# Performance work log

Measured on AMD Instinct MI355X. Metric: run time of the kernel, lower is better.

The kernel has to match this reference:

```python
import jax, jax.numpy as jnp
import numpy as np

S = 4          # number of species / per-species sub-modules
CUTOFF = 5.2


def _routed_mlp(feat, W, b, species_, activate=True):
    # Species-routed MLP: equivalent to per-species index_select -> m_i -> index_add.
    # Compute all species branches vectorized, then select with one-hot mask.
    h = jnp.einsum('ni,sio->nso', feat, W) + b            # [N, S, out]
    if activate:
        h = jax.nn.gelu(h)
    onehot = jax.nn.one_hot(species_, S, dtype=feat.dtype)  # [N, S]; -1 -> all-zero row
    return jnp.einsum('nso,ns->no', h, onehot)            # [N, out]


def _smooth_cutoff(d, rc):
    x = jnp.clip(d / rc, 0.0, 1.0 - 1e-6)
    f = jnp.exp(1.0 - 1.0 / (1.0 - x * x))
    return jnp.where(d < rc, f, 0.0)


def setup_inputs() -> dict:
    key = jax.random.key(0)
    ks = jax.random.split(key, 12)
    B, A, AEV, MO, NO, P = 256, 128, 1008, 256, 128, 262144
    N = B * A
    FIN = MO + NO  # 384
    species = jax.random.randint(ks[0], (B, A), 0, S, dtype=jnp.int32)
    aev = jax.random.normal(ks[1], (B, A, AEV), dtype=jnp.float32)
    atom_index12 = jax.random.randint(ks[2], (2, P), 0, N, dtype=jnp.int32)
    distances = jax.random.uniform(ks[3], (P,), dtype=jnp.float32) * CUTOFF
    total_charges = jax.random.randint(ks[4], (B,), -2, 3).astype(jnp.float32)

    def w(k, shape, fan_in):
        return jax.random.normal(k, shape, dtype=jnp.float32) / np.sqrt(fan_in)

    Wm0 = w(ks[5], (S, AEV, MO), AEV); bm0 = jnp.zeros((S, MO), jnp.float32)
    Wn0 = w(ks[6], (S, MO, NO), MO);   bn0 = jnp.zeros((S, NO), jnp.float32)
    Wm1 = w(ks[7], (S, FIN, MO), FIN); bm1 = jnp.zeros((S, MO), jnp.float32)
    Wn1 = w(ks[8], (S, MO, NO), MO);   bn1 = jnp.zeros((S, NO), jnp.float32)
    Wf  = w(ks[9], (S, FIN, 1), FIN);  bf  = jnp.zeros((S, 1), jnp.float32)
    return dict(species=species, aev=aev, atom_index12=atom_index12,
                distances=distances, total_charges=total_charges,
                Wm0=Wm0, bm0=bm0, Wn0=Wn0, bn0=bn0,
                Wm1=Wm1, bm1=bm1, Wn1=Wn1, bn1=bn1,
                Wf=Wf, bf=bf,
                factor=jnp.float32(1.0), prefactor=jnp.float32(1.0))


def reference(species, aev, atom_index12, distances, total_charges,
              Wm0, bm0, Wn0, bn0, Wm1, bm1, Wn1, bn1, Wf, bf,
              factor, prefactor):
    B, A = species.shape
    species_ = species.reshape(-1)                 # [N]
    feat = aev.reshape(-1, aev.shape[-1])          # [N, AEV]

    # ExpDistanceDecay * smooth cutoff, shared by every pass
    decay = (prefactor ** 2) * jnp.exp(-(factor ** 2) * distances) \
            * _smooth_cutoff(distances, CUTOFF)    # [P]
    idx_flat = atom_index12.reshape(-1)            # [2P] scatter targets
    idx_flip = atom_index12[::-1].reshape(-1)      # [2P] gather sources (flipud)
    decay2 = jnp.tile(decay, 2)                    # [2P]

    for (Wm, bm, Wn, bn) in ((Wm0, bm0, Wn0, bn0), (Wm1, bm1, Wn1, bn1)):
        internal = _routed_mlp(feat, Wm, bm, species_)     # [N, MO]
        neigh = _routed_mlp(internal, Wn, bn, species_)    # [N, NO]
        msgs = neigh[idx_flip] * decay2[:, None]           # [2P, NO]
        merged = jnp.zeros_like(neigh).at[idx_flat].add(msgs)
        feat = jnp.concatenate([internal, merged], axis=-1)  # [N, MO+NO]

    pre = _routed_mlp(feat, Wf, bf, species_, activate=False)[:, 0].reshape(B, A)

    dummy_mask = species != -1
    n_real = dummy_mask.sum(-1, keepdims=True).astype(pre.dtype)
    charges = pre + (total_charges - pre.sum(-1))[:, None] / n_real
    charges = jnp.where(dummy_mask, charges, 0.0)
    return species, charges, pre
```

## Files before the change

kernel.cpp:

```cpp
#include <hip/hip_runtime.h>
#include <hip/hip_bf16.h>
#include <math.h>

constexpr int S_  = 4;
constexpr int MO  = 256;
constexpr int NO  = 128;
constexpr int FIN = 384;
#define CUTOFF_F 5.2f

typedef short bf16x8 __attribute__((ext_vector_type(8)));
typedef float f32x16 __attribute__((ext_vector_type(16)));

__device__ __forceinline__ float gelu_tanh(float x) {
    float u = 0.7978845608028654f * (x + 0.044715f * x * x * x);
    return 0.5f * x * (1.0f + tanhf(u));
}
__device__ __forceinline__ unsigned short f2bf(float x) {
    unsigned u = __float_as_uint(x);
    u = (u + 0x7fffu + ((u >> 16) & 1u)) >> 16;
    return (unsigned short)u;
}
__device__ __forceinline__ float bf2f(unsigned short h) {
    return __uint_as_float(((unsigned)h) << 16);
}
__device__ __forceinline__ float decay_of(float d, float fa, float pf) {
    float x = fminf(fmaxf(d / CUTOFF_F, 0.0f), 1.0f - 1e-6f);
    float f = expf(1.0f - 1.0f / (1.0f - x * x));
    float w = (d < CUTOFF_F) ? f : 0.0f;
    return pf * pf * expf(-(fa * fa) * d) * w;
}

__global__ void species_hist(const int* __restrict__ sp, int* __restrict__ bhist, int N) {
    __shared__ int h[S_];
    int t = threadIdx.x, b = blockIdx.x;
    if (t < S_) h[t] = 0;
    __syncthreads();
    int i = b * 256 + t;
    if (i < N) {
        int s = sp[i];
        if (s >= 0 && s < S_) atomicAdd(&h[s], 1);
    }
    __syncthreads();
    if (t < S_) bhist[b * 4 + t] = h[t];
}
__global__ void species_scan(const int* __restrict__ bhist, int* __restrict__ cnt,
                             int* __restrict__ pbase, int nb) {
    if (threadIdx.x != 0) return;
    int tot[S_];
    for (int s = 0; s < S_; ++s) {
        int sum = 0;
        for (int b = 0; b < nb; ++b) sum += bhist[b * 4 + s];
        tot[s] = sum;
    }
    int off = 0;
    for (int s = 0; s < S_; ++s) { cnt[s] = tot[s]; cnt[4 + s] = off; off += tot[s]; }
    for (int s = 0; s < S_; ++s) {
        int run = cnt[4 + s];
        for (int b = 0; b < nb; ++b) { pbase[b * 4 + s] = run; run += bhist[b * 4 + s]; }
    }
}
__global__ void species_fill(const int* __restrict__ sp, const int* __restrict__ pbase,
                             int* __restrict__ perm, int N) {
    __shared__ int cur[S_];
    int t = threadIdx.x, b = blockIdx.x;
    if (t < S_) cur[t] = pbase[b * 4 + t];
    __syncthreads();
    int i = b * 256 + t;
    if (i < N) {
        int s = sp[i];
        if (s >= 0 && s < S_) {
            int pos = atomicAdd(&cur[s], 1);
            perm[pos] = i;
        }
    }
}

__global__ void edge_count(const int* __restrict__ ai, int* __restrict__ degree, int P2) {
    int e = blockIdx.x * blockDim.x + threadIdx.x;
    if (e < P2) atomicAdd(&degree[ai[e]], 1);
}
__global__ void scan_rowptr(const int* __restrict__ degree, int* __restrict__ rowptr,
                            int* __restrict__ cursor, int N) {
    __shared__ int lds[1024];
    int t = threadIdx.x;
    int per = N / 1024;
    int base = t * per;
    int sum = 0;
    for (int i = 0; i < per; ++i) sum += degree[base + i];
    lds[t] = sum;
    __syncthreads();
    int v = sum;
    for (int ofs = 1; ofs < 1024; ofs <<= 1) {
        int add = (t >= ofs) ? lds[t - ofs] : 0;
        __syncthreads();
        v += add;
        lds[t] = v;
        __syncthreads();
    }
    int run = v - sum;
    for (int i = 0; i < per; ++i) {
        int d = degree[base + i];
        rowptr[base + i] = run;
        cursor[base + i] = run;
        run += d;
    }
    if (t == 1023) rowptr[N] = run;
}
__global__ void edge_fill(const int* __restrict__ ai, const float* __restrict__ dist,
                          const float* __restrict__ fa_, const float* __restrict__ pf_,
                          int* __restrict__ cursor, int* __restrict__ col,
                          float* __restrict__ wgt, int P) {
    int e = blockIdx.x * blockDim.x + threadIdx.x;
    if (e >= 2 * P) return;
    int p = (e < P) ? e : e - P;
    int dst = ai[e];
    int src = (e < P) ? ai[P + p] : ai[p];
    int pos = atomicAdd(&cursor[dst], 1);
    col[pos] = src;
    wgt[pos] = decay_of(dist[p], fa_[0], pf_[0]);
}

__global__ void cast_aev(const float* __restrict__ in, unsigned short* __restrict__ outb, int total4) {
    int i = blockIdx.x * blockDim.x + threadIdx.x;
    if (i >= total4) return;
    float4 v = ((const float4*)in)[i];
    ushort4 o; o.x = f2bf(v.x); o.y = f2bf(v.y); o.z = f2bf(v.z); o.w = f2bf(v.w);
    ((ushort4*)outb)[i] = o;
}

__global__ void transpose_cast(const float* __restrict__ W, unsigned short* __restrict__ Wt,
                               int K, int NC) {
    __shared__ float tile[32][33];
    int s = blockIdx.z;
    int nb = blockIdx.x * 32, kb = blockIdx.y * 32;
    int tx = threadIdx.x & 31, ty = threadIdx.x >> 5;
    const float* Wb = W + (size_t)s * K * NC;
    unsigned short* Wo = Wt + (size_t)s * NC * K;
#pragma unroll
    for (int i = 0; i < 4; ++i) {
        int k = kb + ty + i * 8;
        tile[ty + i * 8][tx] = (k < K) ? Wb[(size_t)k * NC + nb + tx] : 0.0f;
    }
    __syncthreads();
#pragma unroll
    for (int i = 0; i < 4; ++i) {
        int n = nb + ty + i * 8;
        int k = kb + tx;
        if (k < K) Wo[(size_t)n * K + k] = f2bf(tile[tx][ty + i * 8]);
    }
}

template<int K, int NC, bool ACT>
__launch_bounds__(256, 2)
__global__ void mfma_gemm(const unsigned short* __restrict__ A, int lda,
                          const unsigned short* __restrict__ Wt,
                          const float* __restrict__ bias,
                          unsigned short* __restrict__ C, int ldc,
                          const int* __restrict__ cnt, const int* __restrict__ perm) {
    const int s = blockIdx.z;
    const int count = cnt[s];
    const int row0 = blockIdx.y * 64;
    if (row0 >= count) return;
    const int off = cnt[4 + s];
    const int c0 = blockIdx.x * 128;

    __shared__ unsigned short As[64 * 40];
    __shared__ unsigned short Bs[128 * 40];
    __shared__ int rix[64];

    const int t = threadIdx.x;
    const int lane = t & 63, wave = t >> 6;
    const int wm = wave >> 1, wn = wave & 1;
    const int l31 = lane & 31, lhi = lane >> 5;

    if (t < 64) {
        int ri = row0 + t;
        rix[t] = (ri < count) ? perm[off + ri] : -1;
    }
    __syncthreads();

    const int ra = t >> 2, qa = t & 3;
    const int rbr = t >> 1, hb = t & 1;
    const int gA = rix[ra];
    const unsigned short* Arow = (gA >= 0) ? (A + (size_t)gA * lda) : nullptr;
    const unsigned short* wrow = Wt + ((size_t)s * NC + c0 + rbr) * K;

    f32x16 acc0 = {}, acc1 = {};
    const uint4 z4 = {0, 0, 0, 0};

    for (int k0 = 0; k0 < K; k0 += 32) {
        const int ka = k0 + qa * 8;
        uint4 av = z4;
        if (ka < K && Arow) av = *(const uint4*)(Arow + ka);
        const int kb = k0 + hb * 16;
        uint4 b0 = z4, b1 = z4;
        if (kb < K) {
            const uint4* q = (const uint4*)(wrow + kb);
            b0 = q[0]; b1 = q[1];
        }
        __syncthreads();
        *(uint4*)(&As[ra * 40 + qa * 8]) = av;
        *(uint4*)(&Bs[rbr * 40 + hb * 16])     = b0;
        *(uint4*)(&Bs[rbr * 40 + hb * 16 + 8]) = b1;
        __syncthreads();
#pragma unroll
        for (int ks = 0; ks < 2; ++ks) {
            const int ch = (ks * 2 + lhi) * 8;
            bf16x8 fa  = *(const bf16x8*)(&As[(wm * 32 + l31) * 40 + ch]);
            bf16x8 fb0 = *(const bf16x8*)(&Bs[(wn * 64 +  0 + l31) * 40 + ch]);
            bf16x8 fb1 = *(const bf16x8*)(&Bs[(wn * 64 + 32 + l31) * 40 + ch]);
            acc0 = __builtin_amdgcn_mfma_f32_32x32x16_bf16(fa, fb0, acc0, 0, 0, 0);
            acc1 = __builtin_amdgcn_mfma_f32_32x32x16_bf16(fa, fb1, acc1, 0, 0, 0);
        }
    }

    const float* bp = bias + s * NC;
    auto store = [&](const f32x16& vv, int fn) {
        int col = c0 + wn * 64 + fn * 32 + l31;
        float bia = bp[col];
#pragma unroll
        for (int reg = 0; reg < 16; ++reg) {
            int frow = (reg & 3) + 8 * (reg >> 2) + 4 * lhi;
            int r = wm * 32 + frow;
            int g = rix[r];
            if (g >= 0) {
                float x = vv[reg] + bia;
                if (ACT) x = gelu_tanh(x);
                C[(size_t)g * ldc + col] = f2bf(x);
            }
        }
    };
    store(acc0, 0); store(acc1, 1);
}

template<int K, bool ACT>
__launch_bounds__(256, 2)
__global__ void mfma_gemm32(const unsigned short* __restrict__ A, int lda,
                            const unsigned short* __restrict__ Wt,
                            const float* __restrict__ bias,
                            unsigned short* __restrict__ C, int ldc,
                            const int* __restrict__ cnt, const int* __restrict__ perm) {
    const int s = blockIdx.z;
    const int count = cnt[s];
    const int row0 = blockIdx.y * 32;
    if (row0 >= count) return;
    const int off = cnt[4 + s];
    constexpr int NC = 128;

    __shared__ unsigned short As[32 * 40];
    __shared__ unsigned short Bs[128 * 40];
    __shared__ int rix[32];

    const int t = threadIdx.x;
    const int lane = t & 63, wave = t >> 6;
    const int l31 = lane & 31, lhi = lane >> 5;

    if (t < 32) {
        int ri = row0 + t;
        rix[t] = (ri < count) ? perm[off + ri] : -1;
    }
    __syncthreads();

    const int ra = t >> 3, qa = t & 7;
    const int rbr = t >> 1, hb = t & 1;
    const int gA = rix[ra];
    const unsigned short* Arow = (gA >= 0) ? (A + (size_t)gA * lda) : nullptr;
    const unsigned short* wrow = Wt + ((size_t)s * NC + rbr) * K;

    f32x16 acc = {};
    const uint4 z4 = {0, 0, 0, 0};
    const uint2 z2 = {0, 0};

    for (int k0 = 0; k0 < K; k0 += 32) {
        const int ka = k0 + qa * 4;
        uint2 av = z2;
        if (ka < K && Arow) av = *(const uint2*)(Arow + ka);
        const int kb = k0 + hb * 16;
        uint4 b0 = z4, b1 = z4;
        if (kb < K) {
            const uint4* q = (const uint4*)(wrow + kb);
            b0 = q[0]; b1 = q[1];
        }
        __syncthreads();
        *(uint2*)(&As[ra * 40 + qa * 4]) = av;
        *(uint4*)(&Bs[rbr * 40 + hb * 16])     = b0;
        *(uint4*)(&Bs[rbr * 40 + hb * 16 + 8]) = b1;
        __syncthreads();
#pragma unroll
        for (int ks = 0; ks < 2; ++ks) {
            const int ch = (ks * 2 + lhi) * 8;
            bf16x8 fa = *(const bf16x8*)(&As[l31 * 40 + ch]);
            bf16x8 fb = *(const bf16x8*)(&Bs[(wave * 32 + l31) * 40 + ch]);
            acc = __builtin_amdgcn_mfma_f32_32x32x16_bf16(fa, fb, acc, 0, 0, 0);
        }
    }

    const float* bp = bias + s * NC;
    int col = wave * 32 + l31;
    float bia = bp[col];
#pragma unroll
    for (int reg = 0; reg < 16; ++reg) {
        int frow = (reg & 3) + 8 * (reg >> 2) + 4 * lhi;
        int g = rix[frow];
        if (g >= 0) {
            float x = acc[reg] + bia;
            if (ACT) x = gelu_tanh(x);
            C[(size_t)g * ldc + col] = f2bf(x);
        }
    }
}

__global__ void gather_rows0(const unsigned short* __restrict__ neigh,
                             const int* __restrict__ rowptr, const int* __restrict__ col,
                             const float* __restrict__ wgt,
                             unsigned short* __restrict__ featout) {
    int row = blockIdx.x * 4 + (threadIdx.x >> 6);
    int lane = threadIdx.x & 63;
    int b = rowptr[row], e = rowptr[row + 1];
    int j = lane * 2;
    float a0 = 0.f, a1 = 0.f, c0 = 0.f, c1 = 0.f;
    int i = b;
    for (; i + 3 < e; i += 4) {
        int s0 = col[i], s1 = col[i + 1], s2 = col[i + 2], s3 = col[i + 3];
        float w0 = wgt[i], w1 = wgt[i + 1], w2 = wgt[i + 2], w3 = wgt[i + 3];
        unsigned p0 = *(const unsigned*)(neigh + (size_t)s0 * NO + j);
        unsigned p1 = *(const unsigned*)(neigh + (size_t)s1 * NO + j);
        unsigned p2 = *(const unsigned*)(neigh + (size_t)s2 * NO + j);
        unsigned p3 = *(const unsigned*)(neigh + (size_t)s3 * NO + j);
        a0 += bf2f((unsigned short)(p0 & 0xffffu)) * w0 + bf2f((unsigned short)(p2 & 0xffffu)) * w2;
        a1 += bf2f((unsigned short)(p0 >> 16)) * w0 + bf2f((unsigned short)(p2 >> 16)) * w2;
        c0 += bf2f((unsigned short)(p1 & 0xffffu)) * w1 + bf2f((unsigned short)(p3 & 0xffffu)) * w3;
        c1 += bf2f((unsigned short)(p1 >> 16)) * w1 + bf2f((unsigned short)(p3 >> 16)) * w3;
    }
    for (; i < e; ++i) {
        int s0 = col[i];
        float w0 = wgt[i];
        unsigned p0 = *(const unsigned*)(neigh + (size_t)s0 * NO + j);
        a0 += bf2f((unsigned short)(p0 & 0xffffu)) * w0;
        a1 += bf2f((unsigned short)(p0 >> 16)) * w0;
    }
    a0 += c0; a1 += c1;
    unsigned short o0 = f2bf(a0), o1 = f2bf(a1);
    *(unsigned*)(featout + (size_t)row * FIN + MO + j) = ((unsigned)o1 << 16) | (unsigned)o0;
}

__global__ void gather_final(const unsigned short* __restrict__ neigh,
                             const int* __restrict__ rowptr, const int* __restrict__ col,
                             const float* __restrict__ wgt,
                             const unsigned short* __restrict__ int1,
                             const float* __restrict__ Wf, const float* __restrict__ bfb,
                             const int* __restrict__ species, float* __restrict__ out, int N) {
    int w = blockIdx.x * 4 + (threadIdx.x >> 6);
    int lane = threadIdx.x & 63;
    int s = species[w];
    float acc = 0.0f;
    if (s >= 0) {
        const float* wp = Wf + (size_t)s * FIN;
        int b = rowptr[w], e = rowptr[w + 1];
        int j = lane * 2;
        float a0 = 0.f, a1 = 0.f, c0 = 0.f, c1 = 0.f;
        int i = b;
        for (; i + 3 < e; i += 4) {
            int s0 = col[i], s1 = col[i + 1], s2 = col[i + 2], s3 = col[i + 3];
            float w0 = wgt[i], w1 = wgt[i + 1], w2 = wgt[i + 2], w3 = wgt[i + 3];
            unsigned p0 = *(const unsigned*)(neigh + (size_t)s0 * NO + j);
            unsigned p1 = *(const unsigned*)(neigh + (size_t)s1 * NO + j);
            unsigned p2 = *(const unsigned*)(neigh + (size_t)s2 * NO + j);
            unsigned p3 = *(const unsigned*)(neigh + (size_t)s3 * NO + j);
            a0 += bf2f((unsigned short)(p0 & 0xffffu)) * w0 + bf2f((unsigned short)(p2 & 0xffffu)) * w2;
            a1 += bf2f((unsigned short)(p0 >> 16)) * w0 + bf2f((unsigned short)(p2 >> 16)) * w2;
            c0 += bf2f((unsigned short)(p1 & 0xffffu)) * w1 + bf2f((unsigned short)(p3 & 0xffffu)) * w3;
            c1 += bf2f((unsigned short)(p1 >> 16)) * w1 + bf2f((unsigned short)(p3 >> 16)) * w3;
        }
        for (; i < e; ++i) {
            int s0 = col[i];
            float w0 = wgt[i];
            unsigned p0 = *(const unsigned*)(neigh + (size_t)s0 * NO + j);
            a0 += bf2f((unsigned short)(p0 & 0xffffu)) * w0;
            a1 += bf2f((unsigned short)(p0 >> 16)) * w0;
        }
        a0 += c0; a1 += c1;
        acc = a0 * wp[MO + j] + a1 * wp[MO + j + 1];
        const unsigned short* ip = int1 + (size_t)w * MO + lane * 4;
        ushort4 iv = *(const ushort4*)ip;
        const float* wq = wp + lane * 4;
        acc += bf2f(iv.x) * wq[0] + bf2f(iv.y) * wq[1] + bf2f(iv.z) * wq[2] + bf2f(iv.w) * wq[3];
    }
    for (int o = 32; o > 0; o >>= 1) acc += __shfl_down(acc, o, 64);
    if (lane == 0) {
        float pre = (s >= 0) ? (acc + bfb[s]) : 0.0f;
        out[2 * (size_t)N + w] = pre;
        out[w] = (float)s;
    }
}

__global__ void charges_kernel(const float* __restrict__ pre_buf, const int* __restrict__ species,
                               const float* __restrict__ tc, float* __restrict__ out, int N, int A) {
    int b = blockIdx.x;
    int a = threadIdx.x;
    int idx = b * A + a;
    float pre = pre_buf[idx];
    int sp = species[idx];
    bool mask = (sp != -1);
    float v = pre;
    int c = mask ? 1 : 0;
    for (int o = 32; o > 0; o >>= 1) {
        v += __shfl_down(v, o, 64);
        c += __shfl_down(c, o, 64);
    }
    __shared__ float ssum[2];
    __shared__ int scnt[2];
    int wid = threadIdx.x >> 6;
    if ((threadIdx.x & 63) == 0) { ssum[wid] = v; scnt[wid] = c; }
    __syncthreads();
    float total = ssum[0] + ssum[1];
    int nreal = scnt[0] + scnt[1];
    float ch = pre + (tc[b] - total) / (float)max(nreal, 1);
    out[(size_t)N + idx] = mask ? ch : 0.0f;
}

extern "C" void kernel_launch(void* const* d_in, const int* in_sizes, int n_in,
                              void* d_out, int out_size, void* d_ws, size_t ws_size,
                              hipStream_t stream) {
    const int*   species = (const int*)d_in[0];
    const float* aev     = (const float*)d_in[1];
    const int*   ai      = (const int*)d_in[2];
    const float* dist    = (const float*)d_in[3];
    const float* tc      = (const float*)d_in[4];
    const float* Wm0 = (const float*)d_in[5];  const float* bm0 = (const float*)d_in[6];
    const float* Wn0 = (const float*)d_in[7];  const float* bn0 = (const float*)d_in[8];
    const float* Wm1 = (const float*)d_in[9];  const float* bm1 = (const float*)d_in[10];
    const float* Wn1 = (const float*)d_in[11]; const float* bn1 = (const float*)d_in[12];
    const float* Wf  = (const float*)d_in[13]; const float* bf  = (const float*)d_in[14];
    const float* factor    = (const float*)d_in[15];
    const float* prefactor = (const float*)d_in[16];

    const int N   = in_sizes[0];
    const int AEV = in_sizes[1] / N;
    const int P   = in_sizes[3];
    const int B   = in_sizes[4];
    const int A   = N / B;

    float* out = (float*)d_out;

    char* base = (char*)d_ws;
    size_t o = 0;
    auto take = [&](size_t bytes) -> char* {
        o = (o + 255) & ~(size_t)255;
        char* p = base + o; o += bytes; return p;
    };
    unsigned short* feat1_bf = (unsigned short*)take((size_t)N * FIN * 2);
    unsigned short* int1_bf  = (unsigned short*)take((size_t)N * MO * 2);
    char* region             = take((size_t)N * AEV * 2);
    unsigned short* aev_bf   = (unsigned short*)region;
    unsigned short* neigh_bf = (unsigned short*)region;
    size_t roff = ((size_t)N * NO * 2 + 255) & ~(size_t)255;
    int* rowptr = (int*)(region + roff);  roff += (size_t)(N + 1) * 4; roff = (roff + 255) & ~(size_t)255;
    int* cursor = (int*)(region + roff);  roff += (size_t)N * 4;       roff = (roff + 255) & ~(size_t)255;
    int* degree = (int*)(region + roff);  roff += (size_t)N * 4;       roff = (roff + 255) & ~(size_t)255;
    int* ecol   = (int*)(region + roff);  roff += (size_t)2 * P * 4;   roff = (roff + 255) & ~(size_t)255;
    float* ewgt = (float*)(region + roff);
    unsigned short* Wm0t = (unsigned short*)take((size_t)S_ * MO * AEV * 2);
    unsigned short* Wn0t = (unsigned short*)take((size_t)S_ * NO * MO * 2);
    unsigned short* Wm1t = (unsigned short*)take((size_t)S_ * MO * FIN * 2);
    unsigned short* Wn1t = (unsigned short*)take((size_t)S_ * NO * MO * 2);
    int* perm  = (int*)take((size_t)N * 4);
    int* cnt   = (int*)take(64);
    const int nb = (N + 255) / 256;
    int* bhist = (int*)take((size_t)nb * 4 * 4);
    int* pbase = (int*)take((size_t)nb * 4 * 4);

    species_hist<<<nb, 256, 0, stream>>>(species, bhist, N);
    species_scan<<<1, 64, 0, stream>>>(bhist, cnt, pbase, nb);
    species_fill<<<nb, 256, 0, stream>>>(species, pbase, perm, N);

    const int tot4 = N * (AEV / 4);
    cast_aev<<<(tot4 + 255) / 256, 256, 0, stream>>>(aev, aev_bf, tot4);
    transpose_cast<<<dim3(MO / 32, (AEV + 31) / 32, S_), 256, 0, stream>>>(Wm0, Wm0t, AEV, MO);
    transpose_cast<<<dim3(NO / 32, MO / 32, S_), 256, 0, stream>>>(Wn0, Wn0t, MO, NO);
    transpose_cast<<<dim3(MO / 32, FIN / 32, S_), 256, 0, stream>>>(Wm1, Wm1t, FIN, MO);
    transpose_cast<<<dim3(NO / 32, MO / 32, S_), 256, 0, stream>>>(Wn1, Wn1t, MO, NO);

    const int rb  = (N + 63) / 64;
    const int rb32 = (N + 31) / 32;

    mfma_gemm<1008, 256, true><<<dim3(2, rb, S_), 256, 0, stream>>>(
        aev_bf, AEV, Wm0t, bm0, feat1_bf, FIN, cnt, perm);

    hipMemsetAsync(degree, 0, (size_t)N * 4, stream);
    edge_count<<<(2 * P + 255) / 256, 256, 0, stream>>>(ai, degree, 2 * P);
    scan_rowptr<<<1, 1024, 0, stream>>>(degree, rowptr, cursor, N);
    edge_fill<<<(2 * P + 255) / 256, 256, 0, stream>>>(ai, dist, factor, prefactor,
                                                       cursor, ecol, ewgt, P);

    mfma_gemm32<256, true><<<dim3(1, rb32, S_), 256, 0, stream>>>(
        feat1_bf, FIN, Wn0t, bn0, neigh_bf, NO, cnt, perm);
    gather_rows0<<<N / 4, 256, 0, stream>>>(neigh_bf, rowptr, ecol, ewgt, feat1_bf);

    mfma_gemm<384, 256, true><<<dim3(2, rb, S_), 256, 0, stream>>>(
        feat1_bf, FIN, Wm1t, bm1, int1_bf, MO, cnt, perm);
    mfma_gemm32<256, true><<<dim3(1, rb32, S_), 256, 0, stream>>>(
        int1_bf, MO, Wn1t, bn1, neigh_bf, NO, cnt, perm);

    gather_final<<<N / 4, 256, 0, stream>>>(
        neigh_bf, rowptr, ecol, ewgt, int1_bf, Wf, bf, species, out, N);
    charges_kernel<<<B, A, 0, stream>>>(out + 2 * (size_t)N, species, tc, out, N, A);
}
```

Measured before the change: 610.9 us.

## Store all activations in species-sorted padded row order to drop indirect GEMM rows

Rows are permuted once into species-sorted order, with each species segment padded to a multiple of 64, while AEV is cast to bf16. From then on the GEMMs read contiguous rows and pick the species from the tile's offset, with no per-row perm indirection, and the grid drops its per-species z dimension so no blocks exit early. The edge CSR is rebuilt in permuted indices, and the final kernel scatters results back to original atom order. This removes scattered row gathers and wasted blocks, at the cost of an extra inverse-permutation array, padded buffers and extra memsets.

```diff
diff --git a/kernel.cpp b/kernel.cpp
--- a/kernel.cpp
+++ b/kernel.cpp
@@ -53,14 +53,19 @@
         tot[s] = sum;
     }
     int off = 0;
-    for (int s = 0; s < S_; ++s) { cnt[s] = tot[s]; cnt[4 + s] = off; off += tot[s]; }
+    for (int s = 0; s < S_; ++s) {
+        cnt[s] = tot[s];
+        cnt[4 + s] = off;
+        off += ((tot[s] + 63) / 64) * 64;
+    }
+    cnt[8] = off;
     for (int s = 0; s < S_; ++s) {
         int run = cnt[4 + s];
         for (int b = 0; b < nb; ++b) { pbase[b * 4 + s] = run; run += bhist[b * 4 + s]; }
     }
 }
 __global__ void species_fill(const int* __restrict__ sp, const int* __restrict__ pbase,
-                             int* __restrict__ perm, int N) {
+                             int* __restrict__ perm, int* __restrict__ inv_perm, int N) {
     __shared__ int cur[S_];
     int t = threadIdx.x, b = blockIdx.x;
     if (t < S_) cur[t] = pbase[b * 4 + t];
@@ -71,19 +76,40 @@
         if (s >= 0 && s < S_) {
             int pos = atomicAdd(&cur[s], 1);
             perm[pos] = i;
-        }
-    }
-}
-
-__global__ void edge_count(const int* __restrict__ ai, int* __restrict__ degree, int P2) {
+            inv_perm[i] = pos;
+        }
+    }
+}
+
+__global__ void cast_gather(const float* __restrict__ aev, const int* __restrict__ perm,
+                            unsigned short* __restrict__ outb, int AEV) {
+    int row = blockIdx.x;
+    int t = threadIdx.x;
+    if (t * 4 >= AEV) return;
+    int atom = perm[row];
+    ushort4 o;
+    if (atom >= 0) {
+        float4 v = *(const float4*)(aev + (size_t)atom * AEV + t * 4);
+        o.x = f2bf(v.x); o.y = f2bf(v.y); o.z = f2bf(v.z); o.w = f2bf(v.w);
+    } else {
+        o.x = o.y = o.z = o.w = 0;
+    }
+    *(ushort4*)(outb + (size_t)row * AEV + t * 4) = o;
+}
+
+__global__ void edge_count(const int* __restrict__ ai, const int* __restrict__ inv_perm,
+                           int* __restrict__ degree, int P2) {
     int e = blockIdx.x * blockDim.x + threadIdx.x;
-    if (e < P2) atomicAdd(&degree[ai[e]], 1);
+    if (e < P2) {
+        int d = inv_perm[ai[e]];
+        if (d >= 0) atomicAdd(&degree[d], 1);
+    }
 }
 __global__ void scan_rowptr(const int* __restrict__ degree, int* __restrict__ rowptr,
-                            int* __restrict__ cursor, int N) {
+                            int* __restrict__ cursor, int NSCAN) {
     __shared__ int lds[1024];
     int t = threadIdx.x;
-    int per = N / 1024;
+    int per = NSCAN / 1024;
     int base = t * per;
     int sum = 0;
     for (int i = 0; i < per; ++i) sum += degree[base + i];
@@ -104,28 +130,22 @@
         cursor[base + i] = run;
         run += d;
     }
-    if (t == 1023) rowptr[N] = run;
+    if (t == 1023) rowptr[NSCAN] = run;
 }
 __global__ void edge_fill(const int* __restrict__ ai, const float* __restrict__ dist,
                           const float* __restrict__ fa_, const float* __restrict__ pf_,
+                          const int* __restrict__ inv_perm,
                           int* __restrict__ cursor, int* __restrict__ col,
                           float* __restrict__ wgt, int P) {
     int e = blockIdx.x * blockDim.x + threadIdx.x;
     if (e >= 2 * P) return;
     int p = (e < P) ? e : e - P;
-    int dst = ai[e];
-    int src = (e < P) ? ai[P + p] : ai[p];
+    int dst = inv_perm[ai[e]];
+    if (dst < 0) return;
+    int src = inv_perm[(e < P) ? ai[P + p] : ai[p]];
     int pos = atomicAdd(&cursor[dst], 1);
-    col[pos] = src;
-    wgt[pos] = decay_of(dist[p], fa_[0], pf_[0]);
-}
-
-__global__ void cast_aev(const float* __restrict__ in, unsigned short* __restrict__ outb, int total4) {
-    int i = blockIdx.x * blockDim.x + threadIdx.x;
-    if (i >= total4) return;
-    float4 v = ((const float4*)in)[i];
-    ushort4 o; o.x = f2bf(v.x); o.y = f2bf(v.y); o.z = f2bf(v.z); o.w = f2bf(v.w);
-    ((ushort4*)outb)[i] = o;
+    col[pos] = (src >= 0) ? src : 0;
+    wgt[pos] = (src >= 0) ? decay_of(dist[p], fa_[0], pf_[0]) : 0.0f;
 }
 
 __global__ void transpose_cast(const float* __restrict__ W, unsigned short* __restrict__ Wt,
@@ -156,33 +176,23 @@
                           const unsigned short* __restrict__ Wt,
                           const float* __restrict__ bias,
                           unsigned short* __restrict__ C, int ldc,
-                          const int* __restrict__ cnt, const int* __restrict__ perm) {
-    const int s = blockIdx.z;
-    const int count = cnt[s];
+                          const int* __restrict__ cnt) {
     const int row0 = blockIdx.y * 64;
-    if (row0 >= count) return;
-    const int off = cnt[4 + s];
+    if (row0 >= cnt[8]) return;
+    const int s = (row0 >= cnt[5]) + (row0 >= cnt[6]) + (row0 >= cnt[7]);
     const int c0 = blockIdx.x * 128;
 
     __shared__ unsigned short As[64 * 40];
     __shared__ unsigned short Bs[128 * 40];
-    __shared__ int rix[64];
 
     const int t = threadIdx.x;
     const int lane = t & 63, wave = t >> 6;
     const int wm = wave >> 1, wn = wave & 1;
     const int l31 = lane & 31, lhi = lane >> 5;
 
-    if (t < 64) {
-        int ri = row0 + t;
-        rix[t] = (ri < count) ? perm[off + ri] : -1;
-    }
-    __syncthreads();
-
     const int ra = t >> 2, qa = t & 3;
     const int rbr = t >> 1, hb = t & 1;
-    const int gA = rix[ra];
-    const unsigned short* Arow = (gA >= 0) ? (A + (size_t)gA * lda) : nullptr;
+    const unsigned short* Arow = A + (size_t)(row0 + ra) * lda;
     const unsigned short* wrow = Wt + ((size_t)s * NC + c0 + rbr) * K;
 
     f32x16 acc0 = {}, acc1 = {};
@@ -191,7 +201,7 @@
     for (int k0 = 0; k0 < K; k0 += 32) {
         const int ka = k0 + qa * 8;
         uint4 av = z4;
-        if (ka < K && Arow) av = *(const uint4*)(Arow + ka);
+        if (ka < K) av = *(const uint4*)(Arow + ka);
         const int kb = k0 + hb * 16;
         uint4 b0 = z4, b1 = z4;
         if (kb < K) {
@@ -221,13 +231,10 @@
 #pragma unroll
         for (int reg = 0; reg < 16; ++reg) {
             int frow = (reg & 3) + 8 * (reg >> 2) + 4 * lhi;
-            int r = wm * 32 + frow;
-            int g = rix[r];
-            if (g >= 0) {
-                float x = vv[reg] + bia;
-                if (ACT) x = gelu_tanh(x);
-                C[(size_t)g * ldc + col] = f2bf(x);
-            }
+            int r = row0 + wm * 32 + frow;
+            float x = vv[reg] + bia;
+            if (ACT) x = gelu_tanh(x);
+            C[(size_t)r * ldc + col] = f2bf(x);
         }
     };
     store(acc0, 0); store(acc1, 1);
@@ -239,32 +246,22 @@
                             const unsigned short* __restrict__ Wt,
                             const float* __restrict__ bias,
                             unsigned short* __restrict__ C, int ldc,
-                            const int* __restrict__ cnt, const int* __restrict__ perm) {
-    const int s = blockIdx.z;
-    const int count = cnt[s];
+                            const int* __restrict__ cnt) {
     const int row0 = blockIdx.y * 32;
-    if (row0 >= count) return;
-    const int off = cnt[4 + s];
+    if (row0 >= cnt[8]) return;
+    const int s = (row0 >= cnt[5]) + (row0 >= cnt[6]) + (row0 >= cnt[7]);
     constexpr int NC = 128;
 
     __shared__ unsigned short As[32 * 40];
     __shared__ unsigned short Bs[128 * 40];
-    __shared__ int rix[32];
 
     const int t = threadIdx.x;
     const int lane = t & 63, wave = t >> 6;
     const int l31 = lane & 31, lhi = lane >> 5;
 
-    if (t < 32) {
-        int ri = row0 + t;
-        rix[t] = (ri < count) ? perm[off + ri] : -1;
-    }
-    __syncthreads();
-
     const int ra = t >> 3, qa = t & 7;
     const int rbr = t >> 1, hb = t & 1;
-    const int gA = rix[ra];
-    const unsigned short* Arow = (gA >= 0) ? (A + (size_t)gA * lda) : nullptr;
+    const unsigned short* Arow = A + (size_t)(row0 + ra) * lda;
     const unsigned short* wrow = Wt + ((size_t)s * NC + rbr) * K;
 
     f32x16 acc = {};
@@ -274,7 +271,7 @@
     for (int k0 = 0; k0 < K; k0 += 32) {
         const int ka = k0 + qa * 4;
         uint2 av = z2;
-        if (ka < K && Arow) av = *(const uint2*)(Arow + ka);
+        if (ka < K) av = *(const uint2*)(Arow + ka);
         const int kb = k0 + hb * 16;
         uint4 b0 = z4, b1 = z4;
         if (kb < K) {
@@ -301,12 +298,10 @@
 #pragma unroll
     for (int reg = 0; reg < 16; ++reg) {
         int frow = (reg & 3) + 8 * (reg >> 2) + 4 * lhi;
-        int g = rix[frow];
-        if (g >= 0) {
-            float x = acc[reg] + bia;
-            if (ACT) x = gelu_tanh(x);
-            C[(size_t)g * ldc + col] = f2bf(x);
-        }
+        int r = row0 + frow;
+        float x = acc[reg] + bia;
+        if (ACT) x = gelu_tanh(x);
+        C[(size_t)r * ldc + col] = f2bf(x);
     }
 }
 
@@ -348,11 +343,15 @@
                              const int* __restrict__ rowptr, const int* __restrict__ col,
                              const float* __restrict__ wgt,
                              const unsigned short* __restrict__ int1,
+                             const int* __restrict__ perm,
+                             const int* __restrict__ species,
                              const float* __restrict__ Wf, const float* __restrict__ bfb,
-                             const int* __restrict__ species, float* __restrict__ out, int N) {
+                             float* __restrict__ out, int N) {
     int w = blockIdx.x * 4 + (threadIdx.x >> 6);
     int lane = threadIdx.x & 63;
-    int s = species[w];
+    int atom = perm[w];
+    if (atom < 0) return;
+    int s = species[atom];
     float acc = 0.0f;
     if (s >= 0) {
         const float* wp = Wf + (size_t)s * FIN;
@@ -389,8 +388,8 @@
     for (int o = 32; o > 0; o >>= 1) acc += __shfl_down(acc, o, 64);
     if (lane == 0) {
         float pre = (s >= 0) ? (acc + bfb[s]) : 0.0f;
-        out[2 * (size_t)N + w] = pre;
-        out[w] = (float)s;
+        out[2 * (size_t)N + atom] = pre;
+        out[atom] = (float)s;
     }
 }
 
@@ -441,6 +440,9 @@
     const int B   = in_sizes[4];
     const int A   = N / B;
 
+    const int NPAD  = N + 256;
+    const int NSCAN = ((NPAD + 1023) / 1024) * 1024;
+
     float* out = (float*)d_out;
 
     char* base = (char*)d_ws;
@@ -449,60 +451,62 @@
         o = (o + 255) & ~(size_t)255;
         char* p = base + o; o += bytes; return p;
     };
-    unsigned short* feat1_bf = (unsigned short*)take((size_t)N * FIN * 2);
-    unsigned short* int1_bf  = (unsigned short*)take((size_t)N * MO * 2);
-    char* region             = take((size_t)N * AEV * 2);
+    unsigned short* feat1_bf = (unsigned short*)take((size_t)NPAD * FIN * 2);
+    unsigned short* int1_bf  = (unsigned short*)take((size_t)NPAD * MO * 2);
+    char* region             = take((size_t)NPAD * AEV * 2);
     unsigned short* aev_bf   = (unsigned short*)region;
     unsigned short* neigh_bf = (unsigned short*)region;
-    size_t roff = ((size_t)N * NO * 2 + 255) & ~(size_t)255;
-    int* rowptr = (int*)(region + roff);  roff += (size_t)(N + 1) * 4; roff = (roff + 255) & ~(size_t)255;
-    int* cursor = (int*)(region + roff);  roff += (size_t)N * 4;       roff = (roff + 255) & ~(size_t)255;
-    int* degree = (int*)(region + roff);  roff += (size_t)N * 4;       roff = (roff + 255) & ~(size_t)255;
-    int* ecol   = (int*)(region + roff);  roff += (size_t)2 * P * 4;   roff = (roff + 255) & ~(size_t)255;
+    size_t roff = ((size_t)NPAD * NO * 2 + 255) & ~(size_t)255;
+    int* rowptr = (int*)(region + roff);  roff += (size_t)(NSCAN + 1) * 4; roff = (roff + 255) & ~(size_t)255;
+    int* cursor = (int*)(region + roff);  roff += (size_t)NSCAN * 4;       roff = (roff + 255) & ~(size_t)255;
+    int* degree = (int*)(region + roff);  roff += (size_t)NSCAN * 4;       roff = (roff + 255) & ~(size_t)255;
+    int* ecol   = (int*)(region + roff);  roff += (size_t)2 * P * 4;       roff = (roff + 255) & ~(size_t)255;
     float* ewgt = (float*)(region + roff);
     unsigned short* Wm0t = (unsigned short*)take((size_t)S_ * MO * AEV * 2);
     unsigned short* Wn0t = (unsigned short*)take((size_t)S_ * NO * MO * 2);
     unsigned short* Wm1t = (unsigned short*)take((size_t)S_ * MO * FIN * 2);
     unsigned short* Wn1t = (unsigned short*)take((size_t)S_ * NO * MO * 2);
-    int* perm  = (int*)take((size_t)N * 4);
-    int* cnt   = (int*)take(64);
+    int* perm     = (int*)take((size_t)NPAD * 4);
+    int* inv_perm = (int*)take((size_t)N * 4);
+    int* cnt      = (int*)take(64);
     const int nb = (N + 255) / 256;
     int* bhist = (int*)take((size_t)nb * 4 * 4);
     int* pbase = (int*)take((size_t)nb * 4 * 4);
 
+    hipMemsetAsync(perm, 0xFF, (size_t)NPAD * 4, stream);
+    hipMemsetAsync(inv_perm, 0xFF, (size_t)N * 4, stream);
     species_hist<<<nb, 256, 0, stream>>>(species, bhist, N);
     species_scan<<<1, 64, 0, stream>>>(bhist, cnt, pbase, nb);
-    species_fill<<<nb, 256, 0, stream>>>(species, pbase, perm, N);
-
-    const int tot4 = N * (AEV / 4);
-    cast_aev<<<(tot4 + 255) / 256, 256, 0, stream>>>(aev, aev_bf, tot4);
+    species_fill<<<nb, 256, 0, stream>>>(species, pbase, perm, inv_perm, N);
+
+    cast_gather<<<NPAD, 256, 0, stream>>>(aev, perm, aev_bf, AEV);
     transpose_cast<<<dim3(MO / 32, (AEV + 31) / 32, S_), 256, 0, stream>>>(Wm0, Wm0t, AEV, MO);
     transpose_cast<<<dim3(NO / 32, MO / 32, S_), 256, 0, stream>>>(Wn0, Wn0t, MO, NO);
     transpose_cast<<<dim3(MO / 32, FIN / 32, S_), 256, 0, stream>>>(Wm1, Wm1t, FIN, MO);
     transpose_cast<<<dim3(NO / 32, MO / 32, S_), 256, 0, stream>>>(Wn1, Wn1t, MO, NO);
 
-    const int rb  = (N + 63) / 64;
-    const int rb32 = (N + 31) / 32;
-
-    mfma_gemm<1008, 256, true><<<dim3(2, rb, S_), 256, 0, stream>>>(
-        aev_bf, AEV, Wm0t, bm0, feat1_bf, FIN, cnt, perm);
-
-    hipMemsetAsync(degree, 0, (size_t)N * 4, stream);
-    edge_count<<<(2 * P + 255) / 256, 256, 0, stream>>>(ai, degree, 2 * P);
-    scan_rowptr<<<1, 1024, 0, stream>>>(degree, rowptr, cursor, N);
+    const int T64 = NPAD / 64;
+    const int T32 = NPAD / 32;
+
+    mfma_gemm<1008, 256, true><<<dim3(2, T64), 256, 0, stream>>>(
+        aev_bf, AEV, Wm0t, bm0, feat1_bf, FIN, cnt);
+
+    hipMemsetAsync(degree, 0, (size_t)NSCAN * 4, stream);
+    edge_count<<<(2 * P + 255) / 256, 256, 0, stream>>>(ai, inv_perm, degree, 2 * P);
+    scan_rowptr<<<1, 1024, 0, stream>>>(degree, rowptr, cursor, NSCAN);
     edge_fill<<<(2 * P + 255) / 256, 256, 0, stream>>>(ai, dist, factor, prefactor,
-                                                       cursor, ecol, ewgt, P);
-
-    mfma_gemm32<256, true><<<dim3(1, rb32, S_), 256, 0, stream>>>(
-        feat1_bf, FIN, Wn0t, bn0, neigh_bf, NO, cnt, perm);
-    gather_rows0<<<N / 4, 256, 0, stream>>>(neigh_bf, rowptr, ecol, ewgt, feat1_bf);
-
-    mfma_gemm<384, 256, true><<<dim3(2, rb, S_), 256, 0, stream>>>(
-        feat1_bf, FIN, Wm1t, bm1, int1_bf, MO, cnt, perm);
-    mfma_gemm32<256, true><<<dim3(1, rb32, S_), 256, 0, stream>>>(
-        int1_bf, MO, Wn1t, bn1, neigh_bf, NO, cnt, perm);
-
-    gather_final<<<N / 4, 256, 0, stream>>>(
-        neigh_bf, rowptr, ecol, ewgt, int1_bf, Wf, bf, species, out, N);
+                                                       inv_perm, cursor, ecol, ewgt, P);
+
+    mfma_gemm32<256, true><<<dim3(1, T32), 256, 0, stream>>>(
+        feat1_bf, FIN, Wn0t, bn0, neigh_bf, NO, cnt);
+    gather_rows0<<<NPAD / 4, 256, 0, stream>>>(neigh_bf, rowptr, ecol, ewgt, feat1_bf);
+
+    mfma_gemm<384, 256, true><<<dim3(2, T64), 256, 0, stream>>>(
+        feat1_bf, FIN, Wm1t, bm1, int1_bf, MO, cnt);
+    mfma_gemm32<256, true><<<dim3(1, T32), 256, 0, stream>>>(
+        int1_bf, MO, Wn1t, bn1, neigh_bf, NO, cnt);
+
+    gather_final<<<NPAD / 4, 256, 0, stream>>>(
+        neigh_bf, rowptr, ecol, ewgt, int1_bf, perm, species, Wf, bf, out, N);
     charges_kernel<<<B, A, 0, stream>>>(out + 2 * (size_t)N, species, tc, out, N, A);
 }
```

New measurement: 600.9 us. About the same (-1.6%).
